# Kernel tuning notes

Hardware: AMD Instinct MI355X
Metric: run time of the kernel (lower is better)

## Reference

```python
import jax, jax.numpy as jnp
import numpy as np

NUM_HEADS = 16
LN_EPS = 1e-5


def setup_inputs() -> dict:
    key = jax.random.key(0)
    ks = jax.random.split(key, 5)
    B, S, H = 32768, 3, 1024
    scale = 1.0 / np.sqrt(H)
    return {
        "slots": jax.random.normal(ks[0], (B, S, H), dtype=jnp.float32),
        "in_proj_w": jax.random.normal(ks[1], (3 * H, H), dtype=jnp.float32) * scale,
        "in_proj_b": jax.random.normal(ks[2], (3 * H,), dtype=jnp.float32) * 0.02,
        "out_w": jax.random.normal(ks[3], (H, H), dtype=jnp.float32) * scale,
        "out_b": jax.random.normal(ks[4], (H,), dtype=jnp.float32) * 0.02,
        "ln_g": jnp.ones((H,), dtype=jnp.float32),
        "ln_b": jnp.zeros((H,), dtype=jnp.float32),
    }


def reference(slots, in_proj_w, in_proj_b, out_w, out_b, ln_g, ln_b):
    # slots: [B, 3, H]. Matches torch nn.MultiheadAttention (batch_first) in eval
    # mode (dropout inactive) followed by residual add + LayerNorm.
    B, S, H = slots.shape
    nh = NUM_HEADS
    dh = H // nh

    # fused QKV projection: torch does x @ in_proj_w.T + in_proj_b
    qkv = jnp.einsum("bsh,eh->bse", slots, in_proj_w) + in_proj_b  # [B,S,3H]
    q, k, v = jnp.split(qkv, 3, axis=-1)

    def heads(t):  # [B,S,H] -> [B,nh,S,dh]
        return t.reshape(B, S, nh, dh).transpose(0, 2, 1, 3)

    q, k, v = heads(q), heads(k), heads(v)

    scores = jnp.einsum("bnqd,bnkd->bnqk", q, k) / jnp.sqrt(jnp.asarray(dh, slots.dtype))
    attn = jax.nn.softmax(scores, axis=-1)  # [B,nh,3,3]
    ctx = jnp.einsum("bnqk,bnkd->bnqd", attn, v)  # [B,nh,3,dh]
    ctx = ctx.transpose(0, 2, 1, 3).reshape(B, S, H)

    attn_out = jnp.einsum("bsh,oh->bso", ctx, out_w) + out_b  # out_proj

    # residual + LayerNorm (dropout is identity at inference)
    y = slots + attn_out
    mu = jnp.mean(y, axis=-1, keepdims=True)
    var = jnp.mean(jnp.square(y - mu), axis=-1, keepdims=True)
    return (y - mu) / jnp.sqrt(var + LN_EPS) * ln_g + ln_b
```

## Files before the change

### kernel.cpp

```cpp
#include <hip/hip_runtime.h>
#include <stdint.h>

typedef unsigned short u16;
typedef float f32x4 __attribute__((ext_vector_type(4)));
typedef short bf16x8 __attribute__((ext_vector_type(8)));

__device__ __forceinline__ u16 f2bu(float f) {
  uint32_t x = __builtin_bit_cast(uint32_t, f);
  x += 0x7fffu + ((x >> 16) & 1u);
  return (u16)(x >> 16);
}
__device__ __forceinline__ float b2f(u16 u) {
  return __builtin_bit_cast(float, (uint32_t)u << 16);
}
__device__ __forceinline__ void gll16(const void* g, void* l) {
  __builtin_amdgcn_global_load_lds(
      (const __attribute__((address_space(1))) void*)g,
      (__attribute__((address_space(3))) void*)l, 16, 0, 0);
}

__global__ __launch_bounds__(256) void cvt_all_kernel(
    const float* __restrict__ s, u16* __restrict__ os, int ns4,
    const float* __restrict__ w1, u16* __restrict__ o1, int n14,
    const float* __restrict__ w2, u16* __restrict__ o2, int n24) {
  const int stride = gridDim.x * 256;
  const int t0 = blockIdx.x * 256 + threadIdx.x;
  for (int i = t0; i < ns4; i += stride) {
    f32x4 f = __builtin_nontemporal_load(&reinterpret_cast<const f32x4*>(s)[i]);
    ushort4 o;
    o.x = f2bu(f.x); o.y = f2bu(f.y); o.z = f2bu(f.z); o.w = f2bu(f.w);
    reinterpret_cast<ushort4*>(os)[i] = o;
  }
  for (int i = t0; i < n14; i += stride) {
    f32x4 f = __builtin_nontemporal_load(&reinterpret_cast<const f32x4*>(w1)[i]);
    ushort4 o;
    o.x = f2bu(f.x); o.y = f2bu(f.y); o.z = f2bu(f.z); o.w = f2bu(f.w);
    reinterpret_cast<ushort4*>(o1)[i] = o;
  }
  for (int i = t0; i < n24; i += stride) {
    f32x4 f = __builtin_nontemporal_load(&reinterpret_cast<const f32x4*>(w2)[i]);
    ushort4 o;
    o.x = f2bu(f.x); o.y = f2bu(f.y); o.z = f2bu(f.z); o.w = f2bu(f.w);
    reinterpret_cast<ushort4*>(o2)[i] = o;
  }
}

__global__ __launch_bounds__(1024, 4) void gemm256_bt_bias(
    const u16* __restrict__ A, const u16* __restrict__ Bw,
    const float* __restrict__ bias, u16* __restrict__ C,
    int N, int K, int lda, int ldc, int ntn) {
  __shared__ u16 lds[2][2][16384];
  const int tid = threadIdx.x;
  const int lane = tid & 63, wid = tid >> 6;
  const int wr = wid >> 2, wc = wid & 3;
  const int fr = lane & 15, kg = lane >> 4;

  const int bid = blockIdx.x;
  const int xcd = bid & 7;
  const int lid = bid >> 3;
  int mt, nt;
  if (ntn == 12) {
    const int super = lid / 12, sub = lid % 12;
    mt = xcd * 48 + (super >> 2) * 4 + sub / 3;
    nt = (super & 3) * 3 + sub % 3;
  } else {
    const int cpx = (int)gridDim.x >> 3;
    const int sid = xcd * cpx + lid;
    mt = sid / ntn;
    nt = sid % ntn;
  }

  const int srow = tid >> 3;
  const int sc8 = (tid & 7) ^ (srow & 7);
  const u16* Ag = A + (size_t)(mt * 256 + srow) * lda + sc8 * 8;
  const u16* Bg = Bw + (size_t)(nt * 256 + srow) * K + sc8 * 8;
  const size_t arstep = (size_t)128 * lda;
  const size_t brstep = (size_t)128 * K;

  const int fx = fr & 7;
  const int aoff = (wr * 64 + fr) * 64;
  const int boff = (wc * 64 + fr) * 64;

  f32x4 acc[4][4];
#pragma unroll
  for (int i = 0; i < 4; i++)
#pragma unroll
    for (int j = 0; j < 4; j++) acc[i][j] = f32x4{0.f, 0.f, 0.f, 0.f};

  const int NT = K >> 6;

#define STAGE(b, kt) do {                                                  \
    const u16* a_ = Ag + (size_t)(kt) * 64;                                \
    const u16* b_ = Bg + (size_t)(kt) * 64;                                \
    gll16(a_,          &lds[(b)][0][wid * 512]);                           \
    gll16(a_ + arstep, &lds[(b)][0][8192 + wid * 512]);                    \
    gll16(b_,          &lds[(b)][1][wid * 512]);                           \
    gll16(b_ + brstep, &lds[(b)][1][8192 + wid * 512]);                    \
  } while (0)

  STAGE(0, 0);
  __syncthreads();

  for (int t = 0; t < NT; t++) {
    const int cur = t & 1;
    if (t + 1 < NT) STAGE(cur ^ 1, t + 1);
    const u16* As = &lds[cur][0][0];
    const u16* Bs = &lds[cur][1][0];
#pragma unroll
    for (int kh = 0; kh < 2; kh++) {
      const int slot3 = ((kh << 2) | kg) ^ fx;
      bf16x8 a[4], b[4];
#pragma unroll
      for (int nj = 0; nj < 4; nj++)
        b[nj] = *(const bf16x8*)&Bs[boff + nj * 1024 + slot3 * 8];
#pragma unroll
      for (int mi = 0; mi < 4; mi++)
        a[mi] = *(const bf16x8*)&As[aoff + mi * 1024 + slot3 * 8];
      __builtin_amdgcn_s_setprio(1);
#pragma unroll
      for (int mi = 0; mi < 4; mi++)
#pragma unroll
        for (int nj = 0; nj < 4; nj++)
          acc[mi][nj] = __builtin_amdgcn_mfma_f32_16x16x32_bf16(
              a[mi], b[nj], acc[mi][nj], 0, 0, 0);
      __builtin_amdgcn_s_setprio(0);
    }
    __syncthreads();
  }
#undef STAGE

  const int crow0 = mt * 256 + wr * 64 + kg * 4;
  const int ccol0 = nt * 256 + wc * 64 + fr;
#pragma unroll
  for (int nj = 0; nj < 4; nj++) {
    const int col = ccol0 + nj * 16;
    const float bb = bias[col];
#pragma unroll
    for (int mi = 0; mi < 4; mi++) {
      const int r0 = crow0 + mi * 16;
      f32x4 v = acc[mi][nj];
#pragma unroll
      for (int r = 0; r < 4; r++)
        C[(size_t)(r0 + r) * ldc + col] = f2bu(v[r] + bb);
    }
  }
}

__global__ __launch_bounds__(256) void attn3_kernel(
    u16* __restrict__ qkv) {
  const int tid = threadIdx.x;
  const int lane = tid & 63, wid = tid >> 6;
  const int nunit = 32768 * 2;
  for (int unit = blockIdx.x * 4 + wid; unit < nunit; unit += gridDim.x * 4) {
    const int b = unit >> 1, hf = unit & 1;
    const int colb = hf * 512 + (lane >> 3) * 64 + (lane & 7) * 8;
    const size_t base = (size_t)b * 9216 + colb;

    float q[3][8], k[3][8], v[3][8];
#pragma unroll
    for (int s = 0; s < 3; s++) {
      bf16x8 uq = __builtin_nontemporal_load(
          (const bf16x8*)(qkv + base + (size_t)s * 3072));
      bf16x8 uk = __builtin_nontemporal_load(
          (const bf16x8*)(qkv + base + (size_t)s * 3072 + 1024));
      bf16x8 uv = __builtin_nontemporal_load(
          (const bf16x8*)(qkv + base + (size_t)s * 3072 + 2048));
#pragma unroll
      for (int e = 0; e < 8; e++) {
        q[s][e] = b2f((u16)uq[e]);
        k[s][e] = b2f((u16)uk[e]);
        v[s][e] = b2f((u16)uv[e]);
      }
    }

    float sc[3][3];
#pragma unroll
    for (int i = 0; i < 3; i++)
#pragma unroll
      for (int j = 0; j < 3; j++) {
        float p = 0.f;
#pragma unroll
        for (int e = 0; e < 8; e++) p += q[i][e] * k[j][e];
        p += __shfl_xor(p, 1);
        p += __shfl_xor(p, 2);
        p += __shfl_xor(p, 4);
        sc[i][j] = p;
      }

    float o[3][8];
#pragma unroll
    for (int i = 0; i < 3; i++) {
      float mx = fmaxf(sc[i][0], fmaxf(sc[i][1], sc[i][2]));
      float e0 = __expf((sc[i][0] - mx) * 0.125f);
      float e1 = __expf((sc[i][1] - mx) * 0.125f);
      float e2 = __expf((sc[i][2] - mx) * 0.125f);
      float inv = 1.f / (e0 + e1 + e2);
      e0 *= inv; e1 *= inv; e2 *= inv;
#pragma unroll
      for (int e = 0; e < 8; e++)
        o[i][e] = e0 * v[0][e] + e1 * v[1][e] + e2 * v[2][e];
    }

#pragma unroll
    for (int i = 0; i < 3; i++) {
      bf16x8 ov;
#pragma unroll
      for (int e = 0; e < 8; e++) ov[e] = (short)f2bu(o[i][e]);
      *(bf16x8*)(qkv + base + (size_t)i * 3072 + 1024) = ov;
    }
  }
}

__global__ __launch_bounds__(256) void ln_kernel(
    const u16* __restrict__ slots_bf, const u16* __restrict__ ao,
    const float* __restrict__ g, const float* __restrict__ bvec,
    float* __restrict__ out) {
  const int tid = threadIdx.x;
  const int lane = tid & 63, wid = tid >> 6;
  const int row = blockIdx.x * 4 + wid;
  const size_t rb = (size_t)row * 1024;
  const size_t ab = (size_t)row * 3072;

  float y[16];
  float sum = 0.f, sq = 0.f;
#pragma unroll
  for (int c = 0; c < 2; c++) {
    const int col = c * 512 + lane * 8;
    bf16x8 s8 = __builtin_nontemporal_load((const bf16x8*)(slots_bf + rb + col));
    bf16x8 a8 = __builtin_nontemporal_load((const bf16x8*)(ao + ab + col));
#pragma unroll
    for (int e = 0; e < 8; e++) {
      float yv = b2f((u16)s8[e]) + b2f((u16)a8[e]);
      y[c * 8 + e] = yv;
      sum += yv;
      sq += yv * yv;
    }
  }
#pragma unroll
  for (int m = 1; m < 64; m <<= 1) {
    sum += __shfl_xor(sum, m);
    sq  += __shfl_xor(sq, m);
  }
  const float mu = sum * (1.0f / 1024.0f);
  const float var = sq * (1.0f / 1024.0f) - mu * mu;
  const float rs = rsqrtf(var + 1e-5f);
#pragma unroll
  for (int c = 0; c < 2; c++) {
    const int col = c * 512 + lane * 8;
#pragma unroll
    for (int h = 0; h < 2; h++) {
      const float* gp = g + col + h * 4;
      const float* bp = bvec + col + h * 4;
      f32x4 gg = *reinterpret_cast<const f32x4*>(gp);
      f32x4 bb = *reinterpret_cast<const f32x4*>(bp);
      f32x4 ov;
      ov.x = (y[c * 8 + h * 4 + 0] - mu) * rs * gg.x + bb.x;
      ov.y = (y[c * 8 + h * 4 + 1] - mu) * rs * gg.y + bb.y;
      ov.z = (y[c * 8 + h * 4 + 2] - mu) * rs * gg.z + bb.z;
      ov.w = (y[c * 8 + h * 4 + 3] - mu) * rs * gg.w + bb.w;
      __builtin_nontemporal_store(ov, reinterpret_cast<f32x4*>(out + rb + col + h * 4));
    }
  }
}

extern "C" void kernel_launch(void* const* d_in, const int* in_sizes, int n_in,
                              void* d_out, int out_size, void* d_ws, size_t ws_size,
                              hipStream_t stream) {
  const float* slots = (const float*)d_in[0];
  const float* in_w  = (const float*)d_in[1];
  const float* in_b  = (const float*)d_in[2];
  const float* out_w = (const float*)d_in[3];
  const float* out_b = (const float*)d_in[4];
  const float* ln_g  = (const float*)d_in[5];
  const float* ln_b  = (const float*)d_in[6];
  float* out = (float*)d_out;

  const int M = 32768 * 3;

  char* ws = (char*)d_ws;
  u16* Abf   = (u16*)ws;
  u16* Winb  = (u16*)(ws + 201326592);
  u16* Woutb = (u16*)(ws + 207618048);
  u16* qkv   = (u16*)(ws + 209715200);

  cvt_all_kernel<<<2048, 256, 0, stream>>>(
      slots, Abf, M * 1024 / 4,
      in_w, Winb, 3072 * 1024 / 4,
      out_w, Woutb, 1024 * 1024 / 4);

  gemm256_bt_bias<<<384 * 12, 1024, 0, stream>>>(
      Abf, Winb, in_b, qkv, 3072, 1024, 1024, 3072, 12);

  attn3_kernel<<<2048, 256, 0, stream>>>(qkv);

  gemm256_bt_bias<<<384 * 4, 1024, 0, stream>>>(
      qkv + 1024, Woutb, out_b, qkv, 1024, 1024, 3072, 3072, 4);

  ln_kernel<<<M / 4, 256, 0, stream>>>(Abf, qkv, ln_g, ln_b, out);
}
```

Before: 1.274 ms.

## Triple-buffer A tiles and prefetch two k-steps ahead with partial vmcnt waits

The GEMM now keeps three LDS buffers for the A operand and two for B. A is prefetched two k-iterations ahead and B one ahead. The full __syncthreads drain is replaced by a partial s_waitcnt vmcnt(2) plus s_barrier, so outstanding global-to-LDS loads can overlap compute instead of being drained every iteration. LDS usage grows from 64KB to 80KB per block, which may limit occupancy. The correctness of the vmcnt accounting depends on instruction ordering.

Measured after the change: 1.371 ms. +7.6%, slower.

```diff
diff --git a/kernel.cpp b/kernel.cpp
--- a/kernel.cpp
+++ b/kernel.cpp
@@ -4,6 +4,8 @@
 typedef unsigned short u16;
 typedef float f32x4 __attribute__((ext_vector_type(4)));
 typedef short bf16x8 __attribute__((ext_vector_type(8)));
+
+#define MEMFENCE asm volatile("" ::: "memory")
 
 __device__ __forceinline__ u16 f2bu(float f) {
   uint32_t x = __builtin_bit_cast(uint32_t, f);
@@ -49,7 +51,8 @@
     const u16* __restrict__ A, const u16* __restrict__ Bw,
     const float* __restrict__ bias, u16* __restrict__ C,
     int N, int K, int lda, int ldc, int ntn) {
-  __shared__ u16 lds[2][2][16384];
+  __shared__ u16 ldsA[3][16384];
+  __shared__ u16 ldsB[2][16384];
   const int tid = threadIdx.x;
   const int lane = tid & 63, wid = tid >> 6;
   const int wr = wid >> 2, wc = wid & 3;
@@ -89,23 +92,33 @@
 
   const int NT = K >> 6;
 
-#define STAGE(b, kt) do {                                                  \
+#define STAGE_A(b, kt) do {                                                \
     const u16* a_ = Ag + (size_t)(kt) * 64;                                \
+    gll16(a_,          &ldsA[(b)][wid * 512]);                             \
+    gll16(a_ + arstep, &ldsA[(b)][8192 + wid * 512]);                      \
+  } while (0)
+#define STAGE_B(b, kt) do {                                                \
     const u16* b_ = Bg + (size_t)(kt) * 64;                                \
-    gll16(a_,          &lds[(b)][0][wid * 512]);                           \
-    gll16(a_ + arstep, &lds[(b)][0][8192 + wid * 512]);                    \
-    gll16(b_,          &lds[(b)][1][wid * 512]);                           \
-    gll16(b_ + brstep, &lds[(b)][1][8192 + wid * 512]);                    \
+    gll16(b_,          &ldsB[(b)][wid * 512]);                             \
+    gll16(b_ + brstep, &ldsB[(b)][8192 + wid * 512]);                      \
   } while (0)
 
-  STAGE(0, 0);
-  __syncthreads();
-
+  STAGE_A(0, 0);
+  STAGE_B(0, 0);
+  STAGE_A(1, 1);
+  asm volatile("s_waitcnt vmcnt(2)" ::: "memory");
+  __builtin_amdgcn_s_barrier();
+  MEMFENCE;
+
+  int ab = 0, bb = 0;
   for (int t = 0; t < NT; t++) {
-    const int cur = t & 1;
-    if (t + 1 < NT) STAGE(cur ^ 1, t + 1);
-    const u16* As = &lds[cur][0][0];
-    const u16* Bs = &lds[cur][1][0];
+    if (t + 1 < NT) STAGE_B(bb ^ 1, t + 1);
+    if (t + 2 < NT) {
+      int an = ab + 2; if (an >= 3) an -= 3;
+      STAGE_A(an, t + 2);
+    }
+    const u16* As = &ldsA[ab][0];
+    const u16* Bs = &ldsB[bb][0];
 #pragma unroll
     for (int kh = 0; kh < 2; kh++) {
       const int slot3 = ((kh << 2) | kg) ^ fx;
@@ -125,23 +138,29 @@
               a[mi], b[nj], acc[mi][nj], 0, 0, 0);
       __builtin_amdgcn_s_setprio(0);
     }
-    __syncthreads();
-  }
-#undef STAGE
+    if (t < NT - 2) asm volatile("s_waitcnt vmcnt(2)" ::: "memory");
+    else            asm volatile("s_waitcnt vmcnt(0)" ::: "memory");
+    __builtin_amdgcn_s_barrier();
+    MEMFENCE;
+    ab = (ab == 2) ? 0 : ab + 1;
+    bb ^= 1;
+  }
+#undef STAGE_A
+#undef STAGE_B
 
   const int crow0 = mt * 256 + wr * 64 + kg * 4;
   const int ccol0 = nt * 256 + wc * 64 + fr;
 #pragma unroll
   for (int nj = 0; nj < 4; nj++) {
     const int col = ccol0 + nj * 16;
-    const float bb = bias[col];
+    const float bb2 = bias[col];
 #pragma unroll
     for (int mi = 0; mi < 4; mi++) {
       const int r0 = crow0 + mi * 16;
       f32x4 v = acc[mi][nj];
 #pragma unroll
       for (int r = 0; r < 4; r++)
-        C[(size_t)(r0 + r) * ldc + col] = f2bu(v[r] + bb);
+        C[(size_t)(r0 + r) * ldc + col] = f2bu(v[r] + bb2);
     }
   }
 }
```
